# Kernel tuning notes

Hardware: AMD Instinct MI355X
Metric: run time of the kernel (lower is better)

The kernel has to match this reference:

```python
import jax, jax.numpy as jnp
from jax import lax
import numpy as np

B, IN_DIM, T, L, CONN = 32, 256, 512, 512, 256
LN_EPS = 1e-3  # keras LayerNormalization default


def setup_inputs() -> dict:
    key = jax.random.key(0)
    ks = jax.random.split(key, 16)
    g = lambda k, shape, fan: jax.random.normal(k, shape, jnp.float32) * (2.0 / sum(fan)) ** 0.5
    return {
        "x": jax.random.normal(ks[0], (B, IN_DIM, T), jnp.float32),
        "connectivity": jax.random.normal(ks[1], (B, T, CONN), jnp.float32),
        # RandomFourierFeatures: trainable projection + bias, layer-normalized cos features
        "Wf": g(ks[2], (IN_DIM, L), (IN_DIM, L)),
        "bf": jax.random.uniform(ks[3], (L,), jnp.float32, 0.0, 2.0 * np.pi),
        "gamma": jnp.ones((L,), jnp.float32),
        "beta": jnp.zeros((L,), jnp.float32),
        # input gate
        "Wi": g(ks[4], (L, L), (L, L)),
        "Ri": g(ks[5], (L, L), (L, L)),
        "bi": jnp.zeros((L,), jnp.float32),
        # forget gate
        "Wg": g(ks[6], (L, L), (L, L)),
        "Rg": g(ks[7], (L, L), (L, L)),
        "bg": jnp.zeros((L,), jnp.float32),
        # connectivity Dense projection
        "Wc": g(ks[8], (CONN, L), (CONN, L)),
        "bc": jnp.zeros((L,), jnp.float32),
        # learned initial states (stored squeezed to [L])
        "init_h": g(ks[9], (L,), (1, L)),
        "init_c": g(ks[10], (L,), (1, L)),
    }


def reference(x, connectivity, Wf, bf, gamma, beta, Wi, Ri, bi, Wg, Rg, bg, Wc, bc, init_h, init_c):
    xt = jnp.transpose(x, (0, 2, 1))                      # [B, T, in_dim]
    # random fourier features with layer normalization
    p = jnp.cos(xt @ Wf + bf)                             # [B, T, L]
    mu = jnp.mean(p, axis=-1, keepdims=True)
    var = jnp.var(p, axis=-1, keepdims=True)
    z = gamma * (p - mu) * lax.rsqrt(var + LN_EPS) + beta

    o = jnp.sin(z)                                        # sinusoid output gate
    u = connectivity @ Wc + bc                            # [B, T, L] connectivity injection

    b = x.shape[0]
    # hidden_states[t+1] = z_t in the original, so the recurrent term at step t is z_{t-1}
    h0 = jnp.broadcast_to(init_h, (b, 1, z.shape[-1]))
    z_prev = jnp.concatenate([h0, z[:, :-1, :]], axis=1)  # [B, T, L]

    i = jax.nn.sigmoid(z @ Wi + z_prev @ Ri + bi)
    f = jax.nn.sigmoid(z @ Wg + z_prev @ Rg + bg)
    iu = i * u

    def step(c, fi):
        ft, iut = fi
        c = ft * c + iut
        return c, c

    c0 = jnp.broadcast_to(init_c, (b, z.shape[-1]))
    _, cs = lax.scan(step, c0, (jnp.moveaxis(f, 1, 0), jnp.moveaxis(iu, 1, 0)))
    cs = jnp.moveaxis(cs, 0, 1)                           # [B, T, L]
    h = o * cs
    return jnp.transpose(h, (0, 2, 1))                    # [B, L, T]
```

## Files before the change

kernel.cpp:

```cpp
#include <hip/hip_runtime.h>
#include <hip/hip_bf16.h>

#define NB 32
#define IN_DIM 256
#define NT 512
#define NL 512
#define NCONN 256
#define LN_EPS 1e-3f
#define M_TOT (NB * NT)

typedef __attribute__((ext_vector_type(8))) short short8;
typedef __attribute__((ext_vector_type(4))) float f32x4;

__device__ __forceinline__ void async_copy16(void* lds_dst, const void* g_src) {
    __builtin_amdgcn_global_load_lds(
        (const __attribute__((address_space(1))) unsigned int*)g_src,
        (__attribute__((address_space(3))) unsigned int*)lds_dst, 16, 0, 0);
}

__global__ __launch_bounds__(256) void xprep_transpose(
    const float* __restrict__ x, __hip_bfloat16* __restrict__ Axt)
{
    __shared__ float t[64][65];
    const int tilesPerB = (IN_DIM / 64) * (NT / 64);
    const int b  = blockIdx.x / tilesPerB;
    const int tl = blockIdx.x % tilesPerB;
    const int k0 = (tl / (NT / 64)) * 64;
    const int t0 = (tl % (NT / 64)) * 64;
    const int tid = threadIdx.x;
    const float* src = x + (size_t)b * IN_DIM * NT;
    for (int idx = tid; idx < 4096; idx += 256) {
        const int kk = idx >> 6, tt = idx & 63;
        t[kk][tt] = src[(size_t)(k0 + kk) * NT + t0 + tt];
    }
    __syncthreads();
    for (int idx = tid; idx < 4096; idx += 256) {
        const int tt = idx >> 6, kk = idx & 63;
        Axt[((size_t)b * NT + t0 + tt) * IN_DIM + k0 + kk] =
            __float2bfloat16(t[kk][tt]);
    }
}

__global__ void fill_ihb(const float* __restrict__ init_h,
                         __hip_bfloat16* __restrict__ ihb)
{
    const int l = threadIdx.x;
    ihb[l] = __float2bfloat16(init_h[l]);
}

__global__ __launch_bounds__(512, 2) void k1_mfma_fourier_ln(
    const __hip_bfloat16* __restrict__ Axt,
    const __hip_bfloat16* __restrict__ WfT,
    const float* __restrict__ bf, const float* __restrict__ gamma,
    const float* __restrict__ beta,
    __hip_bfloat16* __restrict__ zb)
{
    constexpr int ABYTES = 64 * 128;
    constexpr int BBYTES = 512 * 128;
    constexpr int NBUFB  = ABYTES + BBYTES;
    __shared__ __align__(16) char lds[2 * NBUFB];
    __shared__ float pS[64][8], pQ[64][8];
    __shared__ float mS[64], rS[64];

    const int tid  = threadIdx.x;
    const int wave = tid >> 6, lane = tid & 63;
    const int m0 = blockIdx.x * 64;

    f32x4 acc[4][4];
#pragma unroll
    for (int mi = 0; mi < 4; mi++)
#pragma unroll
        for (int ni = 0; ni < 4; ni++) acc[mi][ni] = f32x4{0.f, 0.f, 0.f, 0.f};

    const int rowq = tid >> 3;
    const int sswz = ((tid & 7) ^ (rowq & 7)) << 4;
    const char* Ab = (const char*)Axt;
    const char* Bb = (const char*)WfT;

    auto stage = [&](int buf, int kt) {
        const size_t kb = (size_t)kt * 128;
        char* base = lds + buf * NBUFB;
        async_copy16(base + tid * 16,
                     Ab + (size_t)(m0 + rowq) * 512 + kb + sswz);
#pragma unroll
        for (int j = 0; j < 8; j++) {
            const int row = j * 64 + rowq;
            async_copy16(base + ABYTES + (j * 512 + tid) * 16,
                         Bb + (size_t)row * 512 + kb + sswz);
        }
    };

    const int l15 = lane & 15, lq = lane >> 4, l7 = lane & 7;
    int kxB[2];
#pragma unroll
    for (int ks = 0; ks < 2; ks++) kxB[ks] = ((ks * 4 + lq) ^ l7) << 4;

    stage(0, 0);
    int cur = 0;
#pragma unroll 1
    for (int kt = 0; kt < 4; kt++) {
        __syncthreads();
        if (kt + 1 < 4) stage(cur ^ 1, kt + 1);
        const char* sA = lds + cur * NBUFB;
        const char* sB = sA + ABYTES;
#pragma unroll
        for (int ks = 0; ks < 2; ks++) {
            const int kx = kxB[ks];
            short8 a[4], b[4];
#pragma unroll
            for (int mi = 0; mi < 4; mi++)
                a[mi] = *(const short8*)(sA + (size_t)(mi * 16 + l15) * 128 + kx);
#pragma unroll
            for (int ni = 0; ni < 4; ni++)
                b[ni] = *(const short8*)(sB +
                    (size_t)(wave * 64 + ni * 16 + l15) * 128 + kx);
#pragma unroll
            for (int ni = 0; ni < 4; ni++)
#pragma unroll
                for (int mi = 0; mi < 4; mi++)
                    acc[mi][ni] = __builtin_amdgcn_mfma_f32_16x16x32_bf16(
                        a[mi], b[ni], acc[mi][ni], 0, 0, 0);
        }
        cur ^= 1;
    }

    int cg[4]; float bfc[4];
#pragma unroll
    for (int ni = 0; ni < 4; ni++) {
        cg[ni] = wave * 64 + ni * 16 + l15;
        bfc[ni] = bf[cg[ni]];
    }

#pragma unroll
    for (int mi = 0; mi < 4; mi++) {
#pragma unroll
        for (int r = 0; r < 4; r++) {
            float s = 0.f, q = 0.f;
#pragma unroll
            for (int ni = 0; ni < 4; ni++) {
                const float p = __cosf(acc[mi][ni][r] + bfc[ni]);
                s += p; q += p * p;
            }
#pragma unroll
            for (int off = 8; off >= 1; off >>= 1) {
                s += __shfl_xor(s, off);
                q += __shfl_xor(q, off);
            }
            if (l15 == 0) {
                const int row = mi * 16 + lq * 4 + r;
                pS[row][wave] = s;
                pQ[row][wave] = q;
            }
        }
    }
    __syncthreads();
    if (tid < 64) {
        float a = 0.f, qq = 0.f;
#pragma unroll
        for (int w = 0; w < 8; w++) { a += pS[tid][w]; qq += pQ[tid][w]; }
        const float mu = a * (1.0f / NL);
        const float var = qq * (1.0f / NL) - mu * mu;
        mS[tid] = mu;
        rS[tid] = rsqrtf(var + LN_EPS);
    }
    __syncthreads();

    float gm[4], bt[4];
#pragma unroll
    for (int ni = 0; ni < 4; ni++) { gm[ni] = gamma[cg[ni]]; bt[ni] = beta[cg[ni]]; }

#pragma unroll
    for (int mi = 0; mi < 4; mi++) {
#pragma unroll
        for (int r = 0; r < 4; r++) {
            const int row = mi * 16 + lq * 4 + r;
            const int m = m0 + row;
            const float mu = mS[row], rs = rS[row];
#pragma unroll
            for (int ni = 0; ni < 4; ni++) {
                const float p = __cosf(acc[mi][ni][r] + bfc[ni]);
                const float z = gm[ni] * (p - mu) * rs + bt[ni];
                zb[(size_t)m * 512 + cg[ni]] = __float2bfloat16(z);
            }
        }
    }
}

__global__ __launch_bounds__(256) void wconv_transpose(
    const float* __restrict__ src, __hip_bfloat16* __restrict__ dst,
    int K, int N, int lddst, int k_off)
{
    __shared__ float t[64][65];
    const int ntn = N >> 6;
    const int k0 = (blockIdx.x / ntn) << 6;
    const int n0 = (blockIdx.x % ntn) << 6;
    const int tid = threadIdx.x;
    for (int idx = tid; idx < 4096; idx += 256) {
        const int kk = idx >> 6, nn = idx & 63;
        t[kk][nn] = src[(size_t)(k0 + kk) * N + n0 + nn];
    }
    __syncthreads();
    for (int idx = tid; idx < 4096; idx += 256) {
        const int nn = idx >> 6, kk = idx & 63;
        dst[(size_t)(n0 + nn) * lddst + k_off + k0 + kk] = __float2bfloat16(t[kk][nn]);
    }
}

__global__ __launch_bounds__(256) void conv_bf16_vec(
    const float* __restrict__ src, __hip_bfloat16* __restrict__ dst, int n)
{
    const int e = (blockIdx.x * 256 + threadIdx.x) * 4;
    if (e < n) {
        const float4 v = *(const float4*)(src + e);
        dst[e + 0] = __float2bfloat16(v.x);
        dst[e + 1] = __float2bfloat16(v.y);
        dst[e + 2] = __float2bfloat16(v.z);
        dst[e + 3] = __float2bfloat16(v.w);
    }
}

template<int KTOT, int EPI>
__global__ __launch_bounds__(256, 4) void gemm_sb(
    const __hip_bfloat16* __restrict__ A,
    const __hip_bfloat16* __restrict__ B,
    const __hip_bfloat16* __restrict__ ihb,
    const float* __restrict__ bi, const float* __restrict__ bg,
    const float* __restrict__ bc,
    __hip_bfloat16* __restrict__ fb, __hip_bfloat16* __restrict__ ub)
{
    constexpr int NTN = (EPI == 1) ? 8 : 4;
    constexpr int TB  = KTOT / 64;
    __shared__ __align__(16) char lds[32768];

    const int tid  = threadIdx.x;
    const int wave = tid >> 6, lane = tid & 63;
    const int wm = wave >> 1, wn = wave & 1;
    constexpr int CPX = 128 * NTN / 8;
    const int d = blockIdx.x;
    const int L = (d & 7) * CPX + (d >> 3);
    const int m0 = (L / NTN) << 7;
    const int n0 = (L % NTN) << 7;

    f32x4 acc[4][4];
#pragma unroll
    for (int mi = 0; mi < 4; mi++)
#pragma unroll
        for (int ni = 0; ni < 4; ni++) acc[mi][ni] = f32x4{0.f, 0.f, 0.f, 0.f};

    auto stage = [&](int kt) {
#pragma unroll
        for (int j = 0; j < 4; j++) {
            const int i = j * 256 + tid;
            const int r = i >> 3;
            const int sl = (i & 7) ^ (r & 7);
            const int ke = kt * 64 + sl * 8;
            const __hip_bfloat16* srcA;
            if constexpr (EPI == 1) {
                const int m = m0 + r;
                if (ke < 512) {
                    srcA = A + (size_t)m * 512 + ke;
                } else {
                    const int k2 = ke - 512;
                    srcA = ((m & (NT - 1)) == 0) ? (ihb + k2)
                                                 : (A + (size_t)(m - 1) * 512 + k2);
                }
            } else {
                srcA = A + (size_t)(m0 + r) * KTOT + ke;
            }
            async_copy16(lds + i * 16, srcA);
            async_copy16(lds + 16384 + i * 16,
                         B + (size_t)(n0 + r) * KTOT + ke);
        }
    };

    const int l15 = lane & 15, lq = lane >> 4, l7 = lane & 7;
    int kx[2];
#pragma unroll
    for (int ks = 0; ks < 2; ks++) kx[ks] = ((ks * 4 + lq) ^ l7) << 4;

#pragma unroll 1
    for (int kt = 0; kt < TB; kt++) {
        stage(kt);
        __syncthreads();
        const char* sA = lds;
        const char* sB = lds + 16384;
#pragma unroll
        for (int ks = 0; ks < 2; ks++) {
            short8 a[4], b[4];
#pragma unroll
            for (int mi = 0; mi < 4; mi++)
                a[mi] = *(const short8*)(sA +
                    (size_t)(wm * 64 + mi * 16 + l15) * 128 + kx[ks]);
#pragma unroll
            for (int ni = 0; ni < 4; ni++)
                b[ni] = *(const short8*)(sB +
                    (size_t)(wn * 64 + ni * 16 + l15) * 128 + kx[ks]);
#pragma unroll
            for (int ni = 0; ni < 4; ni++)
#pragma unroll
                for (int mi = 0; mi < 4; mi++)
                    acc[mi][ni] = __builtin_amdgcn_mfma_f32_16x16x32_bf16(
                        a[mi], b[ni], acc[mi][ni], 0, 0, 0);
        }
        __syncthreads();
    }

#pragma unroll
    for (int ni = 0; ni < 4; ni++) {
        const int gcol = n0 + wn * 64 + ni * 16 + l15;
        if constexpr (EPI == 0) {
            const float bcl = bc[gcol];
#pragma unroll
            for (int mi = 0; mi < 4; mi++)
#pragma unroll
                for (int r = 0; r < 4; r++) {
                    const int m = m0 + wm * 64 + mi * 16 + lq * 4 + r;
                    ub[(size_t)m * 512 + gcol] =
                        __float2bfloat16(acc[mi][ni][r] + bcl);
                }
        } else {
            if (gcol < 512) {
                const float bil = bi[gcol];
#pragma unroll
                for (int mi = 0; mi < 4; mi++)
#pragma unroll
                    for (int r = 0; r < 4; r++) {
                        const int m = m0 + wm * 64 + mi * 16 + lq * 4 + r;
                        const size_t idx = (size_t)m * 512 + gcol;
                        const float iv =
                            1.f / (1.f + __expf(-(acc[mi][ni][r] + bil)));
                        const float uv = __bfloat162float(ub[idx]);
                        ub[idx] = __float2bfloat16(iv * uv);
                    }
            } else {
                const int l2 = gcol - 512;
                const float bgl = bg[l2];
#pragma unroll
                for (int mi = 0; mi < 4; mi++)
#pragma unroll
                    for (int r = 0; r < 4; r++) {
                        const int m = m0 + wm * 64 + mi * 16 + lq * 4 + r;
                        const float fv =
                            1.f / (1.f + __expf(-(acc[mi][ni][r] + bgl)));
                        fb[(size_t)m * 512 + l2] = __float2bfloat16(fv);
                    }
            }
        }
    }
}

__global__ __launch_bounds__(64) void k3_scan(
    const __hip_bfloat16* __restrict__ zb,
    const __hip_bfloat16* __restrict__ fb,
    const __hip_bfloat16* __restrict__ ub,
    const float* __restrict__ init_c, float* __restrict__ out)
{
    const int b = blockIdx.x >> 3;
    const int l = ((blockIdx.x & 7) << 6) + threadIdx.x;
    float c = init_c[l];

    const __hip_bfloat16* zp = zb + (size_t)b * NT * 512 + l;
    const __hip_bfloat16* fp = fb + (size_t)b * NT * NL + l;
    const __hip_bfloat16* ip = ub + (size_t)b * NT * NL + l;
    float* op = out + ((size_t)b * NL + l) * NT;

    for (int t0 = 0; t0 < NT; t0 += 16) {
        float fv[16], iv[16], zv[16];
#pragma unroll
        for (int j = 0; j < 16; j++) {
            fv[j] = __bfloat162float(fp[(size_t)(t0 + j) * NL]);
            iv[j] = __bfloat162float(ip[(size_t)(t0 + j) * NL]);
            zv[j] = __bfloat162float(zp[(size_t)(t0 + j) * 512]);
        }
        float h[16];
#pragma unroll
        for (int j = 0; j < 16; j++) {
            c = fv[j] * c + iv[j];
            h[j] = __sinf(zv[j]) * c;
        }
        float4* o4 = (float4*)(op + t0);
        o4[0] = make_float4(h[0],  h[1],  h[2],  h[3]);
        o4[1] = make_float4(h[4],  h[5],  h[6],  h[7]);
        o4[2] = make_float4(h[8],  h[9],  h[10], h[11]);
        o4[3] = make_float4(h[12], h[13], h[14], h[15]);
    }
}

extern "C" void kernel_launch(void* const* d_in, const int* in_sizes, int n_in,
                              void* d_out, int out_size, void* d_ws, size_t ws_size,
                              hipStream_t stream)
{
    const float* x      = (const float*)d_in[0];
    const float* conn   = (const float*)d_in[1];
    const float* Wf     = (const float*)d_in[2];
    const float* bfv    = (const float*)d_in[3];
    const float* gamma  = (const float*)d_in[4];
    const float* beta   = (const float*)d_in[5];
    const float* Wi     = (const float*)d_in[6];
    const float* Ri     = (const float*)d_in[7];
    const float* bi     = (const float*)d_in[8];
    const float* Wg     = (const float*)d_in[9];
    const float* Rg     = (const float*)d_in[10];
    const float* bg     = (const float*)d_in[11];
    const float* Wc     = (const float*)d_in[12];
    const float* bc     = (const float*)d_in[13];
    const float* init_h = (const float*)d_in[14];
    const float* init_c = (const float*)d_in[15];

    char* w = (char*)d_ws;
    __hip_bfloat16* zbuf = (__hip_bfloat16*)w;  w += (size_t)M_TOT * 512 * 2;
    __hip_bfloat16* cbuf = (__hip_bfloat16*)w;  w += (size_t)M_TOT * NCONN * 2;
    __hip_bfloat16* fbuf = (__hip_bfloat16*)w;  w += (size_t)M_TOT * NL * 2;
    __hip_bfloat16* ubuf = (__hip_bfloat16*)w;  w += (size_t)M_TOT * NL * 2;
    __hip_bfloat16* xbuf = (__hip_bfloat16*)w;  w += (size_t)M_TOT * IN_DIM * 2;
    __hip_bfloat16* WfT  = (__hip_bfloat16*)w;  w += (size_t)NL * IN_DIM * 2;
    __hip_bfloat16* Btig = (__hip_bfloat16*)w;  w += (size_t)1024 * 1024 * 2;
    __hip_bfloat16* Btc  = (__hip_bfloat16*)w;  w += (size_t)NL * NCONN * 2;
    __hip_bfloat16* ihb  = (__hip_bfloat16*)w;  w += 512 * 2;

    wconv_transpose<<<32, 256, 0, stream>>>(Wf, WfT, 256, 512, 256, 0);
    wconv_transpose<<<64, 256, 0, stream>>>(Wi, Btig, 512, 512, 1024, 0);
    wconv_transpose<<<64, 256, 0, stream>>>(Ri, Btig, 512, 512, 1024, 512);
    wconv_transpose<<<64, 256, 0, stream>>>(Wg, Btig + (size_t)512 * 1024, 512, 512, 1024, 0);
    wconv_transpose<<<64, 256, 0, stream>>>(Rg, Btig + (size_t)512 * 1024, 512, 512, 1024, 512);
    wconv_transpose<<<32, 256, 0, stream>>>(Wc, Btc, 256, 512, 256, 0);
    conv_bf16_vec<<<(M_TOT * NCONN / 4 + 255) / 256, 256, 0, stream>>>(
        conn, cbuf, M_TOT * NCONN);
    xprep_transpose<<<NB * 32, 256, 0, stream>>>(x, xbuf);
    fill_ihb<<<1, 512, 0, stream>>>(init_h, ihb);

    k1_mfma_fourier_ln<<<M_TOT / 64, 512, 0, stream>>>(
        xbuf, WfT, bfv, gamma, beta, zbuf);

    gemm_sb<NCONN, 0><<<M_TOT / 128 * 4, 256, 0, stream>>>(
        cbuf, Btc, nullptr, nullptr, nullptr, bc, nullptr, ubuf);

    gemm_sb<1024, 1><<<M_TOT / 128 * 8, 256, 0, stream>>>(
        zbuf, Btig, ihb, bi, bg, nullptr, fbuf, ubuf);

    k3_scan<<<NB * 8, 64, 0, stream>>>(zbuf, fbuf, ubuf, init_c, (float*)d_out);
}
```

Baseline: 133.0 us.

## Fuse input transpose/convert into Fourier GEMM and connectivity GEMM into input gate

Result: faster. 129.7 us (-2.4%).

```diff
diff --git a/kernel.cpp b/kernel.cpp
--- a/kernel.cpp
+++ b/kernel.cpp
@@ -18,27 +18,9 @@
         (__attribute__((address_space(3))) unsigned int*)lds_dst, 16, 0, 0);
 }
 
-__global__ __launch_bounds__(256) void xprep_transpose(
-    const float* __restrict__ x, __hip_bfloat16* __restrict__ Axt)
-{
-    __shared__ float t[64][65];
-    const int tilesPerB = (IN_DIM / 64) * (NT / 64);
-    const int b  = blockIdx.x / tilesPerB;
-    const int tl = blockIdx.x % tilesPerB;
-    const int k0 = (tl / (NT / 64)) * 64;
-    const int t0 = (tl % (NT / 64)) * 64;
-    const int tid = threadIdx.x;
-    const float* src = x + (size_t)b * IN_DIM * NT;
-    for (int idx = tid; idx < 4096; idx += 256) {
-        const int kk = idx >> 6, tt = idx & 63;
-        t[kk][tt] = src[(size_t)(k0 + kk) * NT + t0 + tt];
-    }
-    __syncthreads();
-    for (int idx = tid; idx < 4096; idx += 256) {
-        const int tt = idx >> 6, kk = idx & 63;
-        Axt[((size_t)b * NT + t0 + tt) * IN_DIM + k0 + kk] =
-            __float2bfloat16(t[kk][tt]);
-    }
+__device__ __forceinline__ ushort f2bf(float f) {
+    unsigned int x = __float_as_uint(f);
+    return (ushort)((x + 0x7FFFu + ((x >> 16) & 1u)) >> 16);
 }
 
 __global__ void fill_ihb(const float* __restrict__ init_h,
@@ -49,7 +31,7 @@
 }
 
 __global__ __launch_bounds__(512, 2) void k1_mfma_fourier_ln(
-    const __hip_bfloat16* __restrict__ Axt,
+    const float* __restrict__ x,
     const __hip_bfloat16* __restrict__ WfT,
     const float* __restrict__ bf, const float* __restrict__ gamma,
     const float* __restrict__ beta,
@@ -65,6 +47,9 @@
     const int tid  = threadIdx.x;
     const int wave = tid >> 6, lane = tid & 63;
     const int m0 = blockIdx.x * 64;
+    const int b  = m0 >> 9;
+    const int t0 = m0 & 511;
+    const float* xb = x + (size_t)b * IN_DIM * NT;
 
     f32x4 acc[4][4];
 #pragma unroll
@@ -74,14 +59,26 @@
 
     const int rowq = tid >> 3;
     const int sswz = ((tid & 7) ^ (rowq & 7)) << 4;
-    const char* Ab = (const char*)Axt;
     const char* Bb = (const char*)WfT;
 
     auto stage = [&](int buf, int kt) {
+        char* base = lds + buf * NBUFB;
+#pragma unroll
+        for (int j = 0; j < 2; j++) {
+            const int ci = j * 512 + tid;
+            const int k  = ci >> 4;
+            const int tc = ci & 15;
+            const float4 v = *(const float4*)(
+                xb + ((size_t)(kt * 64 + k)) * NT + t0 + tc * 4);
+            const ushort h[4] = {f2bf(v.x), f2bf(v.y), f2bf(v.z), f2bf(v.w)};
+            const int sl = k >> 3, kb2 = (k & 7) << 1;
+#pragma unroll
+            for (int e = 0; e < 4; e++) {
+                const int t = tc * 4 + e;
+                *(ushort*)(base + t * 128 + (((sl) ^ (t & 7)) << 4) + kb2) = h[e];
+            }
+        }
         const size_t kb = (size_t)kt * 128;
-        char* base = lds + buf * NBUFB;
-        async_copy16(base + tid * 16,
-                     Ab + (size_t)(m0 + rowq) * 512 + kb + sswz);
 #pragma unroll
         for (int j = 0; j < 8; j++) {
             const int row = j * 64 + rowq;
@@ -206,40 +203,75 @@
     }
 }
 
-__global__ __launch_bounds__(256) void conv_bf16_vec(
-    const float* __restrict__ src, __hip_bfloat16* __restrict__ dst, int n)
-{
-    const int e = (blockIdx.x * 256 + threadIdx.x) * 4;
-    if (e < n) {
-        const float4 v = *(const float4*)(src + e);
-        dst[e + 0] = __float2bfloat16(v.x);
-        dst[e + 1] = __float2bfloat16(v.y);
-        dst[e + 2] = __float2bfloat16(v.z);
-        dst[e + 3] = __float2bfloat16(v.w);
-    }
-}
-
-template<int KTOT, int EPI>
-__global__ __launch_bounds__(256, 4) void gemm_sb(
-    const __hip_bfloat16* __restrict__ A,
-    const __hip_bfloat16* __restrict__ B,
+#define GATES_PRELUDE                                                         \
+    const int tid  = threadIdx.x;                                             \
+    const int wave = tid >> 6, lane = tid & 63;                               \
+    const int wm = wave >> 1, wn = wave & 1;                                  \
+    const int d = blockIdx.x;                                                 \
+    const int L = (d & 7) * 64 + (d >> 3);                                    \
+    const int m0 = (L >> 2) << 7;                                             \
+    const int n0 = (L & 3) << 7;                                              \
+    const int l15 = lane & 15, lq = lane >> 4, l7 = lane & 7;                 \
+    int kx[2];                                                                \
+    kx[0] = (lq ^ l7) << 4;                                                   \
+    kx[1] = ((4 + lq) ^ l7) << 4;
+
+#define STAGE_AZ(kt)                                                          \
+    {                                                                         \
+        _Pragma("unroll")                                                     \
+        for (int j = 0; j < 4; j++) {                                         \
+            const int i = j * 256 + tid;                                      \
+            const int r = i >> 3;                                             \
+            const int sl = (i & 7) ^ (r & 7);                                 \
+            const int ke = (kt) * 64 + sl * 8;                                \
+            const __hip_bfloat16* srcA;                                       \
+            const int m = m0 + r;                                             \
+            if (ke < 512) {                                                   \
+                srcA = Az + (size_t)m * 512 + ke;                             \
+            } else {                                                          \
+                const int k2 = ke - 512;                                      \
+                srcA = ((m & (NT - 1)) == 0) ? (ihb + k2)                     \
+                                             : (Az + (size_t)(m - 1) * 512 + k2); \
+            }                                                                 \
+            async_copy16(lds + i * 16, srcA);                                 \
+            async_copy16(lds + 16384 + i * 16,                                \
+                         Bg + (size_t)(n0 + r) * 1024 + ke);                  \
+        }                                                                     \
+    }
+
+#define COMPUTE_TILE(ACC)                                                     \
+    {                                                                         \
+        const char* sA = lds;                                                 \
+        const char* sB = lds + 16384;                                         \
+        _Pragma("unroll")                                                     \
+        for (int ks = 0; ks < 2; ks++) {                                      \
+            short8 a[4], b[4];                                                \
+            _Pragma("unroll")                                                 \
+            for (int mi = 0; mi < 4; mi++)                                    \
+                a[mi] = *(const short8*)(sA +                                 \
+                    (size_t)(wm * 64 + mi * 16 + l15) * 128 + kx[ks]);        \
+            _Pragma("unroll")                                                 \
+            for (int ni = 0; ni < 4; ni++)                                    \
+                b[ni] = *(const short8*)(sB +                                 \
+                    (size_t)(wn * 64 + ni * 16 + l15) * 128 + kx[ks]);        \
+            _Pragma("unroll")                                                 \
+            for (int ni = 0; ni < 4; ni++)                                    \
+                _Pragma("unroll")                                             \
+                for (int mi = 0; mi < 4; mi++)                                \
+                    ACC[mi][ni] = __builtin_amdgcn_mfma_f32_16x16x32_bf16(    \
+                        a[mi], b[ni], ACC[mi][ni], 0, 0, 0);                  \
+        }                                                                     \
+    }
+
+__global__ __launch_bounds__(256, 4) void gates_f(
+    const __hip_bfloat16* __restrict__ Az,
+    const __hip_bfloat16* __restrict__ Bg,
     const __hip_bfloat16* __restrict__ ihb,
-    const float* __restrict__ bi, const float* __restrict__ bg,
-    const float* __restrict__ bc,
-    __hip_bfloat16* __restrict__ fb, __hip_bfloat16* __restrict__ ub)
-{
-    constexpr int NTN = (EPI == 1) ? 8 : 4;
-    constexpr int TB  = KTOT / 64;
+    const float* __restrict__ bg,
+    __hip_bfloat16* __restrict__ fb)
+{
     __shared__ __align__(16) char lds[32768];
-
-    const int tid  = threadIdx.x;
-    const int wave = tid >> 6, lane = tid & 63;
-    const int wm = wave >> 1, wn = wave & 1;
-    constexpr int CPX = 128 * NTN / 8;
-    const int d = blockIdx.x;
-    const int L = (d & 7) * CPX + (d >> 3);
-    const int m0 = (L / NTN) << 7;
-    const int n0 = (L % NTN) << 7;
+    GATES_PRELUDE
 
     f32x4 acc[4][4];
 #pragma unroll
@@ -247,105 +279,102 @@
 #pragma unroll
         for (int ni = 0; ni < 4; ni++) acc[mi][ni] = f32x4{0.f, 0.f, 0.f, 0.f};
 
-    auto stage = [&](int kt) {
+#pragma unroll 1
+    for (int kt = 0; kt < 16; kt++) {
+        STAGE_AZ(kt)
+        __syncthreads();
+        COMPUTE_TILE(acc)
+        __syncthreads();
+    }
+
+#pragma unroll
+    for (int ni = 0; ni < 4; ni++) {
+        const int gcol = n0 + wn * 64 + ni * 16 + l15;
+        const float bgl = bg[gcol];
+#pragma unroll
+        for (int mi = 0; mi < 4; mi++)
+#pragma unroll
+            for (int r = 0; r < 4; r++) {
+                const int m = m0 + wm * 64 + mi * 16 + lq * 4 + r;
+                const float fv = 1.f / (1.f + __expf(-(acc[mi][ni][r] + bgl)));
+                fb[(size_t)m * 512 + gcol] = __float2bfloat16(fv);
+            }
+    }
+}
+
+__global__ __launch_bounds__(256, 2) void gates_iu(
+    const __hip_bfloat16* __restrict__ Az,
+    const __hip_bfloat16* __restrict__ Bg,
+    const float* __restrict__ conn,
+    const __hip_bfloat16* __restrict__ Btc,
+    const __hip_bfloat16* __restrict__ ihb,
+    const float* __restrict__ bi, const float* __restrict__ bc,
+    __hip_bfloat16* __restrict__ ub)
+{
+    __shared__ __align__(16) char lds[32768];
+    GATES_PRELUDE
+
+    f32x4 accu[4][4];
+#pragma unroll
+    for (int mi = 0; mi < 4; mi++)
+#pragma unroll
+        for (int ni = 0; ni < 4; ni++) accu[mi][ni] = f32x4{0.f, 0.f, 0.f, 0.f};
+
+#pragma unroll 1
+    for (int kt = 0; kt < 4; kt++) {
+#pragma unroll
+        for (int j = 0; j < 8; j++) {
+            const int ci = j * 256 + tid;
+            const int r  = ci >> 4;
+            const int c4 = ci & 15;
+            const float4 v = *(const float4*)(
+                conn + (size_t)(m0 + r) * NCONN + kt * 64 + c4 * 4);
+            ushort4 h;
+            h.x = f2bf(v.x); h.y = f2bf(v.y); h.z = f2bf(v.z); h.w = f2bf(v.w);
+            const int sl = c4 >> 1, half = c4 & 1;
+            *(ushort4*)(lds + r * 128 + ((sl ^ (r & 7)) << 4) + half * 8) = h;
+        }
 #pragma unroll
         for (int j = 0; j < 4; j++) {
             const int i = j * 256 + tid;
             const int r = i >> 3;
             const int sl = (i & 7) ^ (r & 7);
             const int ke = kt * 64 + sl * 8;
-            const __hip_bfloat16* srcA;
-            if constexpr (EPI == 1) {
-                const int m = m0 + r;
-                if (ke < 512) {
-                    srcA = A + (size_t)m * 512 + ke;
-                } else {
-                    const int k2 = ke - 512;
-                    srcA = ((m & (NT - 1)) == 0) ? (ihb + k2)
-                                                 : (A + (size_t)(m - 1) * 512 + k2);
-                }
-            } else {
-                srcA = A + (size_t)(m0 + r) * KTOT + ke;
-            }
-            async_copy16(lds + i * 16, srcA);
             async_copy16(lds + 16384 + i * 16,
-                         B + (size_t)(n0 + r) * KTOT + ke);
-        }
-    };
-
-    const int l15 = lane & 15, lq = lane >> 4, l7 = lane & 7;
-    int kx[2];
-#pragma unroll
-    for (int ks = 0; ks < 2; ks++) kx[ks] = ((ks * 4 + lq) ^ l7) << 4;
+                         Btc + (size_t)(n0 + r) * NCONN + ke);
+        }
+        __syncthreads();
+        COMPUTE_TILE(accu)
+        __syncthreads();
+    }
+
+    f32x4 acc[4][4];
+#pragma unroll
+    for (int mi = 0; mi < 4; mi++)
+#pragma unroll
+        for (int ni = 0; ni < 4; ni++) acc[mi][ni] = f32x4{0.f, 0.f, 0.f, 0.f};
 
 #pragma unroll 1
-    for (int kt = 0; kt < TB; kt++) {
-        stage(kt);
-        __syncthreads();
-        const char* sA = lds;
-        const char* sB = lds + 16384;
-#pragma unroll
-        for (int ks = 0; ks < 2; ks++) {
-            short8 a[4], b[4];
-#pragma unroll
-            for (int mi = 0; mi < 4; mi++)
-                a[mi] = *(const short8*)(sA +
-                    (size_t)(wm * 64 + mi * 16 + l15) * 128 + kx[ks]);
-#pragma unroll
-            for (int ni = 0; ni < 4; ni++)
-                b[ni] = *(const short8*)(sB +
-                    (size_t)(wn * 64 + ni * 16 + l15) * 128 + kx[ks]);
-#pragma unroll
-            for (int ni = 0; ni < 4; ni++)
-#pragma unroll
-                for (int mi = 0; mi < 4; mi++)
-                    acc[mi][ni] = __builtin_amdgcn_mfma_f32_16x16x32_bf16(
-                        a[mi], b[ni], acc[mi][ni], 0, 0, 0);
-        }
+    for (int kt = 0; kt < 16; kt++) {
+        STAGE_AZ(kt)
+        __syncthreads();
+        COMPUTE_TILE(acc)
         __syncthreads();
     }
 
 #pragma unroll
     for (int ni = 0; ni < 4; ni++) {
         const int gcol = n0 + wn * 64 + ni * 16 + l15;
-        if constexpr (EPI == 0) {
-            const float bcl = bc[gcol];
-#pragma unroll
-            for (int mi = 0; mi < 4; mi++)
-#pragma unroll
-                for (int r = 0; r < 4; r++) {
-                    const int m = m0 + wm * 64 + mi * 16 + lq * 4 + r;
-                    ub[(size_t)m * 512 + gcol] =
-                        __float2bfloat16(acc[mi][ni][r] + bcl);
-                }
-        } else {
-            if (gcol < 512) {
-                const float bil = bi[gcol];
-#pragma unroll
-                for (int mi = 0; mi < 4; mi++)
-#pragma unroll
-                    for (int r = 0; r < 4; r++) {
-                        const int m = m0 + wm * 64 + mi * 16 + lq * 4 + r;
-                        const size_t idx = (size_t)m * 512 + gcol;
-                        const float iv =
-                            1.f / (1.f + __expf(-(acc[mi][ni][r] + bil)));
-                        const float uv = __bfloat162float(ub[idx]);
-                        ub[idx] = __float2bfloat16(iv * uv);
-                    }
-            } else {
-                const int l2 = gcol - 512;
-                const float bgl = bg[l2];
-#pragma unroll
-                for (int mi = 0; mi < 4; mi++)
-#pragma unroll
-                    for (int r = 0; r < 4; r++) {
-                        const int m = m0 + wm * 64 + mi * 16 + lq * 4 + r;
-                        const float fv =
-                            1.f / (1.f + __expf(-(acc[mi][ni][r] + bgl)));
-                        fb[(size_t)m * 512 + l2] = __float2bfloat16(fv);
-                    }
-            }
-        }
+        const float bil = bi[gcol], bcl = bc[gcol];
+#pragma unroll
+        for (int mi = 0; mi < 4; mi++)
+#pragma unroll
+            for (int r = 0; r < 4; r++) {
+                const int m = m0 + wm * 64 + mi * 16 + lq * 4 + r;
+                const float iv = 1.f / (1.f + __expf(-(acc[mi][ni][r] + bil)));
+                const float uv = accu[mi][ni][r] + bcl;
+                ub[(size_t)m * 512 + gcol] = __float2bfloat16(iv * uv);
+            }
     }
 }
 
@@ -409,10 +438,8 @@
 
     char* w = (char*)d_ws;
     __hip_bfloat16* zbuf = (__hip_bfloat16*)w;  w += (size_t)M_TOT * 512 * 2;
-    __hip_bfloat16* cbuf = (__hip_bfloat16*)w;  w += (size_t)M_TOT * NCONN * 2;
     __hip_bfloat16* fbuf = (__hip_bfloat16*)w;  w += (size_t)M_TOT * NL * 2;
     __hip_bfloat16* ubuf = (__hip_bfloat16*)w;  w += (size_t)M_TOT * NL * 2;
-    __hip_bfloat16* xbuf = (__hip_bfloat16*)w;  w += (size_t)M_TOT * IN_DIM * 2;
     __hip_bfloat16* WfT  = (__hip_bfloat16*)w;  w += (size_t)NL * IN_DIM * 2;
     __hip_bfloat16* Btig = (__hip_bfloat16*)w;  w += (size_t)1024 * 1024 * 2;
     __hip_bfloat16* Btc  = (__hip_bfloat16*)w;  w += (size_t)NL * NCONN * 2;
@@ -424,19 +451,14 @@
     wconv_transpose<<<64, 256, 0, stream>>>(Wg, Btig + (size_t)512 * 1024, 512, 512, 1024, 0);
     wconv_transpose<<<64, 256, 0, stream>>>(Rg, Btig + (size_t)512 * 1024, 512, 512, 1024, 512);
     wconv_transpose<<<32, 256, 0, stream>>>(Wc, Btc, 256, 512, 256, 0);
-    conv_bf16_vec<<<(M_TOT * NCONN / 4 + 255) / 256, 256, 0, stream>>>(
-        conn, cbuf, M_TOT * NCONN);
-    xprep_transpose<<<NB * 32, 256, 0, stream>>>(x, xbuf);
     fill_ihb<<<1, 512, 0, stream>>>(init_h, ihb);
 
     k1_mfma_fourier_ln<<<M_TOT / 64, 512, 0, stream>>>(
-        xbuf, WfT, bfv, gamma, beta, zbuf);
-
-    gemm_sb<NCONN, 0><<<M_TOT / 128 * 4, 256, 0, stream>>>(
-        cbuf, Btc, nullptr, nullptr, nullptr, bc, nullptr, ubuf);
-
-    gemm_sb<1024, 1><<<M_TOT / 128 * 8, 256, 0, stream>>>(
-        zbuf, Btig, ihb, bi, bg, nullptr, fbuf, ubuf);
+        x, WfT, bfv, gamma, beta, zbuf);
+
+    gates_iu<<<512, 256, 0, stream>>>(zbuf, Btig, conn, Btc, ihb, bi, bc, ubuf);
+
+    gates_f<<<512, 256, 0, stream>>>(zbuf, Btig + (size_t)512 * 1024, ihb, bg, fbuf);
 
     k3_scan<<<NB * 8, 64, 0, stream>>>(zbuf, fbuf, ubuf, init_c, (float*)d_out);
 }
```
